# Optimization experiments

Measured on AMD Instinct MI355X. Metric: run time of the kernel, lower is better.

Reference implementation:

```python
import jax, jax.numpy as jnp
import numpy as np


def _gru_cell(xi, h, w_ih, w_hh, b_ih, b_hh):
    # Faithful torch.nn.GRUCell math (as written in KeyedGRU.get_key_gate.one_step)
    gi = xi @ w_ih.T + b_ih            # [B, 3H]
    gh = h @ w_hh.T + b_hh             # [B, 3H]
    i_r, i_i, i_n = jnp.split(gi, 3, axis=1)
    h_r, h_i, h_n = jnp.split(gh, 3, axis=1)
    resetgate = jax.nn.sigmoid(i_r + h_r)
    inputgate = jax.nn.sigmoid(i_i + h_i)
    newgate = jnp.tanh(i_n + resetgate * h_n)
    hy = newgate + inputgate * (h - newgate)
    return hy, resetgate


def setup_inputs() -> dict:
    key = jax.random.key(0)
    ks = jax.random.split(key, 6)
    B, T, I, H = 64, 2048, 256, 256
    KB, KL = 4, 16
    s = 1.0 / float(np.sqrt(H))
    x = jax.random.normal(ks[0], (B, T, I), jnp.float32)
    wm_key = jax.random.normal(ks[1], (KB, KL, I), jnp.float32)
    weight_ih = jax.random.uniform(ks[2], (3 * H, I), jnp.float32, -s, s)
    weight_hh = jax.random.uniform(ks[3], (3 * H, H), jnp.float32, -s, s)
    bias_ih = jax.random.uniform(ks[4], (3 * H,), jnp.float32, -s, s)
    bias_hh = jax.random.uniform(ks[5], (3 * H,), jnp.float32, -s, s)
    return {"x": x, "wm_key": wm_key, "weight_ih": weight_ih,
            "weight_hh": weight_hh, "bias_ih": bias_ih, "bias_hh": bias_hh}


def reference(x, wm_key, weight_ih, weight_hh, bias_ih, bias_hh):
    B, T, I = x.shape
    H = weight_hh.shape[1]
    dt = x.dtype

    # --- key-gate scan (get_key_gate): collect reset gate per key timestep ---
    kt = jnp.transpose(wm_key, (1, 0, 2))          # [KL, KB, I]
    KL, KB, _ = kt.shape
    kh0 = jnp.zeros((KB, H), dt)                   # hidden_init='zero'

    def kstep(h, xi):
        hy, r = _gru_cell(xi, h, weight_ih, weight_hh, bias_ih, bias_hh)
        return hy, r

    _, rgates = jax.lax.scan(kstep, kh0, kt)       # [KL, KB, H]
    gate_means = rgates.mean(axis=1)               # [KL, H] -- key_gates[i].mean(dim=0)
    # pad with ones for steps i >= key_len (no gating applied there)
    gates_full = jnp.concatenate([gate_means, jnp.ones((T - KL, H), dt)], axis=0)  # [T, H]

    # --- main recurrence (teacher_forcing=True, return_sequences=True) ---
    xt = jnp.transpose(x, (1, 0, 2))               # [T, B, I]
    h0 = jnp.zeros((B, H), dt)

    def step(h, inp):
        xi, g = inp
        hy, _ = _gru_cell(xi, h, weight_ih, weight_hh, bias_ih, bias_hh)
        # NOTE: original appends hy to output BEFORE the key-gate multiply,
        # but carries the gated hidden state forward.
        return hy * g, hy

    _, out = jax.lax.scan(step, h0, (xt, gates_full))  # out: [T, B, H]
    return out
```

## Files before the change

kernel.cpp:

```cpp
#include <hip/hip_runtime.h>

typedef _Float16 f16;
typedef _Float16 half8 __attribute__((ext_vector_type(8)));
typedef _Float16 half2v __attribute__((ext_vector_type(2)));
typedef _Float16 half4 __attribute__((ext_vector_type(4)));
typedef float f32x4 __attribute__((ext_vector_type(4)));
typedef unsigned int uint2v __attribute__((ext_vector_type(2)));
typedef unsigned int u32x4v __attribute__((ext_vector_type(4)));

#define G3 768

__global__ void cvt_f32_f16(const float* __restrict__ in, f16* __restrict__ out, int n) {
  int i = blockIdx.x * blockDim.x + threadIdx.x;
  if (i < n) out[i] = (f16)in[i];
}

__global__ __launch_bounds__(256, 2)
void gi_gemm(const float* __restrict__ A, const f16* __restrict__ W,
             const float* __restrict__ b_ih, const float* __restrict__ b_hh,
             f16* __restrict__ GIri, f16* __restrict__ GIn) {
  const int tid = threadIdx.x;
  const int lane = tid & 63;
  const int w = tid >> 6;
  const int quad = lane >> 4;
  const int lq = lane & 15;
  const int m0 = blockIdx.x * 64;

  __shared__ __align__(16) f16 Al[64 * 264];
  __shared__ __align__(16) f16 Bl[48 * 264];

#pragma unroll
  for (int i = 0; i < 16; ++i) {
    int f = i * 256 + tid;
    int row = f >> 6;
    int c4 = f & 63;
    float4 v = ((const float4*)A)[(size_t)(m0 + row) * 64 + c4];
    half4 hv = {(f16)v.x, (f16)v.y, (f16)v.z, (f16)v.w};
    *(half4*)&Al[row * 264 + c4 * 4] = hv;
  }
  __syncthreads();

  half8 af[8];
#pragma unroll
  for (int kc = 0; kc < 8; ++kc)
    af[kc] = *(half8*)&Al[(w * 16 + lq) * 264 + kc * 32 + quad * 8];

  for (int nc = 0; nc < 16; ++nc) {
    __syncthreads();
    int n0 = nc * 48;
#pragma unroll
    for (int i = 0; i < 6; ++i) {
      int f = i * 256 + tid;
      int row = f >> 5;
      int c8 = f & 31;
      half8 v = ((const half8*)(W + (size_t)(n0 + row) * 256))[c8];
      *(half8*)&Bl[row * 264 + c8 * 8] = v;
    }
    __syncthreads();

    f32x4 acc[3] = {};
#pragma unroll
    for (int kc = 0; kc < 8; ++kc) {
#pragma unroll
      for (int nt = 0; nt < 3; ++nt) {
        half8 bf = *(half8*)&Bl[(nt * 16 + lq) * 264 + kc * 32 + quad * 8];
        acc[nt] = __builtin_amdgcn_mfma_f32_16x16x32_f16(af[kc], bf, acc[nt], 0, 0, 0);
      }
    }
#pragma unroll
    for (int nt = 0; nt < 3; ++nt) {
      int n = n0 + nt * 16 + lq;
      float bv = b_ih[n] + (n < 512 ? b_hh[n] : 0.f);
      int g = n >> 8;
      int u = n & 255;
      int ww = u >> 5, lq16 = u & 15, s = (u >> 4) & 1;
#pragma unroll
      for (int r = 0; r < 4; ++r) {
        int m = m0 + w * 16 + quad * 4 + r;
        float val = acc[nt][r] + bv;
        size_t base = ((size_t)m * 8 + ww) * 16 + lq16;
        if (g < 2) GIri[base * 4 + g * 2 + s] = (f16)val;
        else       GIn[base * 2 + s] = (f16)val;
      }
    }
  }
}

__device__ __forceinline__ float sigf(float x) {
  return __builtin_amdgcn_rcpf(1.f + __expf(-x));
}
__device__ __forceinline__ float tanhf_(float x) {
  return 1.f - 2.f * __builtin_amdgcn_rcpf(__expf(2.f * x) + 1.f);
}

#if defined(__has_builtin)
#if __has_builtin(__builtin_amdgcn_fdot2)
#define FD(a, b, c) __builtin_amdgcn_fdot2(a, b, c, false)
#endif
#endif
#ifndef FD
#define FD(a, b, c) ((c) + (float)(a)[0] * (float)(b)[0] + (float)(a)[1] * (float)(b)[1])
#endif

#define MF(af, bw, c) __builtin_amdgcn_mfma_f32_16x16x32_f16(af, bw, c, 0, 0, 0)

#define LOADW(t6, kc) { \
    const float* wr_ = Whh + (size_t)(((t6 >> 1) * 256) + w * 32 + ((t6 & 1) * 16) + lq) * 256 + (kc * 32 + colb); \
    float4 va_ = *(const float4*)wr_; float4 vb_ = *(const float4*)(wr_ + 4); \
    w##t6##kc = (half8){(f16)va_.x, (f16)va_.y, (f16)va_.z, (f16)va_.w, \
                        (f16)vb_.x, (f16)vb_.y, (f16)vb_.z, (f16)vb_.w}; }

#define LOADW_T6(t6) \
  LOADW(t6, 0) LOADW(t6, 1) LOADW(t6, 2) LOADW(t6, 3) \
  LOADW(t6, 4) LOADW(t6, 5) LOADW(t6, 6) LOADW(t6, 7)

#define UNPACK2(u32, lo, hi) { half2v h2_ = __builtin_bit_cast(half2v, (unsigned int)(u32)); \
                               lo = (float)h2_[0]; hi = (float)h2_[1]; }

#define H2(v4, j) __builtin_bit_cast(half2v, (unsigned int)((v4)[j]))

#define NCHUNK(c) { \
    a0 = MF(f##c##_, w0##c, a0); a1 = MF(f##c##_, w1##c, a1); \
    a2 = MF(f##c##_, w2##c, a2); a3 = MF(f##c##_, w3##c, a3); \
    int no_ = nC0 ^ ((c) << 6); \
    half8 n0_ = *(const half8*)((const char*)n_lds + no_); \
    half8 n1_ = *(const half8*)((const char*)n_lds + no_ + 8192); \
    u32x4v hu_ = __builtin_bit_cast(u32x4v, f##c##_); \
    u32x4v nu0_ = __builtin_bit_cast(u32x4v, n0_); \
    u32x4v nu1_ = __builtin_bit_cast(u32x4v, n1_); \
    an0 = FD(H2(hu_, 0), H2(nu0_, 0), an0); an1 = FD(H2(hu_, 0), H2(nu1_, 0), an1); \
    an0 = FD(H2(hu_, 1), H2(nu0_, 1), an0); an1 = FD(H2(hu_, 1), H2(nu1_, 1), an1); \
    an0 = FD(H2(hu_, 2), H2(nu0_, 2), an0); an1 = FD(H2(hu_, 2), H2(nu1_, 2), an1); \
    an0 = FD(H2(hu_, 3), H2(nu0_, 3), an0); an1 = FD(H2(hu_, 3), H2(nu1_, 3), an1); }

#define RED(x) { \
    int t_ = __builtin_amdgcn_ds_swizzle(__builtin_bit_cast(int, x), 0x401F); \
    x += __builtin_bit_cast(float, t_); \
    t_ = __builtin_amdgcn_ds_bpermute(pidx, __builtin_bit_cast(int, x)); \
    x += __builtin_bit_cast(float, t_); }

#define STEP(tcur, PRI, PN) { \
    const f16* hr_ = &hbuf[(tcur) & 1][0]; \
    half8 f0_ = *(const half8*)(hr_ + 0 * 32 + colb); \
    half8 f1_ = *(const half8*)(hr_ + 1 * 32 + colb); \
    half8 f2_ = *(const half8*)(hr_ + 2 * 32 + colb); \
    half8 f3_ = *(const half8*)(hr_ + 3 * 32 + colb); \
    half8 f4_ = *(const half8*)(hr_ + 4 * 32 + colb); \
    half8 f5_ = *(const half8*)(hr_ + 5 * 32 + colb); \
    half8 f6_ = *(const half8*)(hr_ + 6 * 32 + colb); \
    half8 f7_ = *(const half8*)(hr_ + 7 * 32 + colb); \
    float gr0_, gr1_, gi0_, gi1_, gn0_, gn1_; \
    UNPACK2(PRI[0], gr0_, gr1_); \
    UNPACK2(PRI[1], gi0_, gi1_); \
    UNPACK2(PN, gn0_, gn1_); \
    if ((tcur) + 2 < T) { \
      PRI = *(const uint2v*)(gri + (size_t)((tcur) + 2) * 512); \
      PN = *(const unsigned int*)(gn + (size_t)((tcur) + 2) * 256); \
    } \
    f32x4 a0 = {}, a1 = {}, a2 = {}, a3 = {}; \
    float an0 = 0.f, an1 = 0.f; \
    NCHUNK(0) NCHUNK(1) NCHUNK(2) NCHUNK(3) \
    NCHUNK(4) NCHUNK(5) NCHUNK(6) NCHUNK(7) \
    RED(an0) RED(an1) \
    float rg0_ = sigf(gr0_ + a0[0]); \
    float rg1_ = sigf(gr1_ + a1[0]); \
    float ig0_ = sigf(gi0_ + a2[0]); \
    float ig1_ = sigf(gi1_ + a3[0]); \
    float ng0_ = tanhf_(gn0_ + rg0_ * (bn0 + an0)); \
    float ng1_ = tanhf_(gn1_ + rg1_ * (bn1 + an1)); \
    float hy0_ = ng0_ + ig0_ * (h0 - ng0_); \
    float hy1_ = ng1_ + ig1_ * (h1 - ng1_); \
    if (IS_KEY) { \
      if (quad == 0) { float* o_ = out + ((size_t)(tcur) * nb + b) * 256 + u0; o_[0] = rg0_; o_[16] = rg1_; } \
      h0 = hy0_; h1 = hy1_; \
    } else { \
      if (quad == 0) { float* o_ = out + ((size_t)(tcur) * nb + b) * 256 + u0; o_[0] = hy0_; o_[16] = hy1_; } \
      float gm0_ = 1.f, gm1_ = 1.f; \
      if ((tcur) < 16) { gm0_ = gates[(tcur) * 256 + u0]; gm1_ = gates[(tcur) * 256 + u0 + 16]; } \
      h0 = hy0_ * gm0_; h1 = hy1_ * gm1_; \
    } \
    if (quad == 0) { f16* hw_ = &hbuf[((tcur) + 1) & 1][0]; hw_[u0] = (f16)h0; hw_[u0 + 16] = (f16)h1; } \
    __asm__ volatile("" ::: "memory"); \
    __builtin_amdgcn_s_waitcnt(0xC07F);  \
    __builtin_amdgcn_s_barrier(); \
    __asm__ volatile("" ::: "memory"); }

template <bool IS_KEY>
__global__ __launch_bounds__(512)
__attribute__((amdgpu_waves_per_eu(2, 2)))
void gru_scan(const float* __restrict__ Whh, const float* __restrict__ bhh,
              const f16* __restrict__ GIri, const f16* __restrict__ GIn,
              const float* __restrict__ gates, float* __restrict__ out, int T) {
  const int tid = threadIdx.x;
  const int lane = tid & 63;
  const int w = tid >> 6;
  const int quad = lane >> 4;
  const int lq = lane & 15;
  const int b = blockIdx.x;
  const int nb = gridDim.x;
  const int colb = quad * 8;
  const int u0 = w * 32 + lq;
  const int pidx = (lane ^ 32) << 2;

  __shared__ __align__(16) f16 n_lds[256 * 256];
  __shared__ __align__(16) f16 hbuf[2][256];

  half8 w00, w01, w02, w03, w04, w05, w06, w07;
  half8 w10, w11, w12, w13, w14, w15, w16, w17;
  half8 w20, w21, w22, w23, w24, w25, w26, w27;
  half8 w30, w31, w32, w33, w34, w35, w36, w37;
  LOADW_T6(0) LOADW_T6(1) LOADW_T6(2) LOADW_T6(3)

#pragma unroll 4
  for (int i = 0; i < 16; ++i) {
    int gid = i * 512 + tid;
    int rn = gid >> 5, g = gid & 31;
    const float* p_ = Whh + (size_t)(512 + rn) * 256 + g * 8;
    float4 va = *(const float4*)p_;
    float4 vb = *(const float4*)(p_ + 4);
    half8 hv = {(f16)va.x, (f16)va.y, (f16)va.z, (f16)va.w,
                (f16)vb.x, (f16)vb.y, (f16)vb.z, (f16)vb.w};
    *(half8*)((char*)n_lds + rn * 512 + ((g ^ (rn & 7)) << 4)) = hv;
  }

  if (tid < 256) { hbuf[0][tid] = (f16)0.f; hbuf[1][tid] = (f16)0.f; }

  const int e_ = u0 & 7;
  const int nC0 = u0 * 512 + ((quad ^ (e_ & 3)) << 4) + ((e_ >> 2) << 6);

  float h0 = 0.f, h1 = 0.f;
  const float bn0 = bhh[512 + u0];
  const float bn1 = bhh[512 + u0 + 16];

  const size_t mstart = (size_t)b * T;
  const f16* gri = GIri + ((mstart * 8 + w) * 16 + lq) * 4;
  const f16* gn  = GIn + ((mstart * 8 + w) * 16 + lq) * 2;

  uint2v priA = *(const uint2v*)(gri);
  unsigned int pnA = *(const unsigned int*)(gn);
  uint2v priB = *(const uint2v*)(gri + 512);
  unsigned int pnB = *(const unsigned int*)(gn + 256);

  __syncthreads();

  for (int t = 0; t < T; t += 2) {
    STEP(t, priA, pnA)
    STEP(t + 1, priB, pnB)
  }
}

__global__ void gate_mean(const float* __restrict__ rg, float* __restrict__ g) {
  int i = blockIdx.x * 256 + threadIdx.x;
  int l = i >> 8;
  int j = i & 255;
  float s = 0.f;
#pragma unroll
  for (int kb = 0; kb < 4; ++kb) s += rg[((size_t)l * 4 + kb) * 256 + j];
  g[i] = 0.25f * s;
}

extern "C" void kernel_launch(void* const* d_in, const int* in_sizes, int n_in,
                              void* d_out, int out_size, void* d_ws, size_t ws_size,
                              hipStream_t stream) {
  const float* x      = (const float*)d_in[0];
  const float* wm_key = (const float*)d_in[1];
  const float* w_ih   = (const float*)d_in[2];
  const float* w_hh   = (const float*)d_in[3];
  const float* b_ih   = (const float*)d_in[4];
  const float* b_hh   = (const float*)d_in[5];
  float* out = (float*)d_out;

  char* ws = (char*)d_ws;
  const size_t GIRI_OFF  = 0;
  const size_t GIN_OFF   = GIRI_OFF + 134217728ull;
  const size_t WIH_OFF   = GIN_OFF + 67108864ull;
  const size_t GIKRI_OFF = WIH_OFF + 393216ull;
  const size_t GIKN_OFF  = GIKRI_OFF + 65536ull;
  const size_t RG_OFF    = GIKN_OFF + 32768ull;
  const size_t G_OFF     = RG_OFF + 65536ull;
  f16*   GIri  = (f16*)(ws + GIRI_OFF);
  f16*   GIn   = (f16*)(ws + GIN_OFF);
  f16*   Wih   = (f16*)(ws + WIH_OFF);
  f16*   GIkri = (f16*)(ws + GIKRI_OFF);
  f16*   GIkn  = (f16*)(ws + GIKN_OFF);
  float* rg    = (float*)(ws + RG_OFF);
  float* g     = (float*)(ws + G_OFF);

  cvt_f32_f16<<<dim3(768), dim3(256), 0, stream>>>(w_ih, Wih, G3 * 256);
  gi_gemm<<<dim3(2048), dim3(256), 0, stream>>>(x, Wih, b_ih, b_hh, GIri, GIn);
  gi_gemm<<<dim3(1), dim3(256), 0, stream>>>(wm_key, Wih, b_ih, b_hh, GIkri, GIkn);
  gru_scan<true><<<dim3(4), dim3(512), 0, stream>>>(w_hh, b_hh, GIkri, GIkn, g, rg, 16);
  gate_mean<<<dim3(16), dim3(256), 0, stream>>>(rg, g);
  gru_scan<false><<<dim3(64), dim3(512), 0, stream>>>(w_hh, b_hh, GIri, GIn, g, out, 2048);
}
```

Before: 3.503 ms.

## Move input and new-gate recurrent weights into registers, use packed dot products

The update-gate and new-gate parts of W_hh are now held per lane in registers as half2 pairs. They are combined with the hidden state through scalar dot products plus a cross-lane reduction, where before the update gate used MFMA and the new gate was streamed from a 128 KB LDS copy. This drops the LDS weight reads and the large shared allocation, and reduces MFMA work to the reset gate only. The h-fragment loads are also interleaved with the compute chunks. In exchange it adds 128 VGPRs of weights and more VALU dot-product and reduction instructions on the serial per-step critical path.

```diff
diff --git a/kernel.cpp b/kernel.cpp
--- a/kernel.cpp
+++ b/kernel.cpp
@@ -114,24 +114,35 @@
   LOADW(t6, 0) LOADW(t6, 1) LOADW(t6, 2) LOADW(t6, 3) \
   LOADW(t6, 4) LOADW(t6, 5) LOADW(t6, 6) LOADW(t6, 7)
 
+#define LDW2(arr, grow, u) { \
+    _Pragma("unroll") \
+    for (int c_ = 0; c_ < 8; ++c_) { \
+      const float* p_ = Whh + ((size_t)(grow) * 256 + (u)) * 256 + c_ * 32 + colb; \
+      float4 va_ = *(const float4*)p_; \
+      float4 vb_ = *(const float4*)(p_ + 4); \
+      arr[c_ * 4 + 0] = (half2v){(f16)va_.x, (f16)va_.y}; \
+      arr[c_ * 4 + 1] = (half2v){(f16)va_.z, (f16)va_.w}; \
+      arr[c_ * 4 + 2] = (half2v){(f16)vb_.x, (f16)vb_.y}; \
+      arr[c_ * 4 + 3] = (half2v){(f16)vb_.z, (f16)vb_.w}; \
+    } }
+
 #define UNPACK2(u32, lo, hi) { half2v h2_ = __builtin_bit_cast(half2v, (unsigned int)(u32)); \
                                lo = (float)h2_[0]; hi = (float)h2_[1]; }
 
 #define H2(v4, j) __builtin_bit_cast(half2v, (unsigned int)((v4)[j]))
 
-#define NCHUNK(c) { \
+#define CH(c) { \
     a0 = MF(f##c##_, w0##c, a0); a1 = MF(f##c##_, w1##c, a1); \
-    a2 = MF(f##c##_, w2##c, a2); a3 = MF(f##c##_, w3##c, a3); \
-    int no_ = nC0 ^ ((c) << 6); \
-    half8 n0_ = *(const half8*)((const char*)n_lds + no_); \
-    half8 n1_ = *(const half8*)((const char*)n_lds + no_ + 8192); \
     u32x4v hu_ = __builtin_bit_cast(u32x4v, f##c##_); \
-    u32x4v nu0_ = __builtin_bit_cast(u32x4v, n0_); \
-    u32x4v nu1_ = __builtin_bit_cast(u32x4v, n1_); \
-    an0 = FD(H2(hu_, 0), H2(nu0_, 0), an0); an1 = FD(H2(hu_, 0), H2(nu1_, 0), an1); \
-    an0 = FD(H2(hu_, 1), H2(nu0_, 1), an0); an1 = FD(H2(hu_, 1), H2(nu1_, 1), an1); \
-    an0 = FD(H2(hu_, 2), H2(nu0_, 2), an0); an1 = FD(H2(hu_, 2), H2(nu1_, 2), an1); \
-    an0 = FD(H2(hu_, 3), H2(nu0_, 3), an0); an1 = FD(H2(hu_, 3), H2(nu1_, 3), an1); }
+    half2v h20_ = H2(hu_, 0), h21_ = H2(hu_, 1), h22_ = H2(hu_, 2), h23_ = H2(hu_, 3); \
+    ai0 = FD(h20_, wiA[(c) * 4 + 0], ai0); ai1 = FD(h20_, wiB[(c) * 4 + 0], ai1); \
+    an0 = FD(h20_, wnA[(c) * 4 + 0], an0); an1 = FD(h20_, wnB[(c) * 4 + 0], an1); \
+    ai0 = FD(h21_, wiA[(c) * 4 + 1], ai0); ai1 = FD(h21_, wiB[(c) * 4 + 1], ai1); \
+    an0 = FD(h21_, wnA[(c) * 4 + 1], an0); an1 = FD(h21_, wnB[(c) * 4 + 1], an1); \
+    ai0 = FD(h22_, wiA[(c) * 4 + 2], ai0); ai1 = FD(h22_, wiB[(c) * 4 + 2], ai1); \
+    an0 = FD(h22_, wnA[(c) * 4 + 2], an0); an1 = FD(h22_, wnB[(c) * 4 + 2], an1); \
+    ai0 = FD(h23_, wiA[(c) * 4 + 3], ai0); ai1 = FD(h23_, wiB[(c) * 4 + 3], ai1); \
+    an0 = FD(h23_, wnA[(c) * 4 + 3], an0); an1 = FD(h23_, wnB[(c) * 4 + 3], an1); }
 
 #define RED(x) { \
     int t_ = __builtin_amdgcn_ds_swizzle(__builtin_bit_cast(int, x), 0x401F); \
@@ -141,14 +152,22 @@
 
 #define STEP(tcur, PRI, PN) { \
     const f16* hr_ = &hbuf[(tcur) & 1][0]; \
+    f32x4 a0 = {}, a1 = {}; \
+    float ai0 = 0.f, ai1 = 0.f, an0 = 0.f, an1 = 0.f; \
     half8 f0_ = *(const half8*)(hr_ + 0 * 32 + colb); \
     half8 f1_ = *(const half8*)(hr_ + 1 * 32 + colb); \
     half8 f2_ = *(const half8*)(hr_ + 2 * 32 + colb); \
     half8 f3_ = *(const half8*)(hr_ + 3 * 32 + colb); \
+    CH(0) \
     half8 f4_ = *(const half8*)(hr_ + 4 * 32 + colb); \
+    CH(1) \
     half8 f5_ = *(const half8*)(hr_ + 5 * 32 + colb); \
+    CH(2) \
     half8 f6_ = *(const half8*)(hr_ + 6 * 32 + colb); \
+    CH(3) \
     half8 f7_ = *(const half8*)(hr_ + 7 * 32 + colb); \
+    CH(4) CH(5) CH(6) CH(7) \
+    RED(ai0) RED(ai1) RED(an0) RED(an1) \
     float gr0_, gr1_, gi0_, gi1_, gn0_, gn1_; \
     UNPACK2(PRI[0], gr0_, gr1_); \
     UNPACK2(PRI[1], gi0_, gi1_); \
@@ -157,15 +176,10 @@
       PRI = *(const uint2v*)(gri + (size_t)((tcur) + 2) * 512); \
       PN = *(const unsigned int*)(gn + (size_t)((tcur) + 2) * 256); \
     } \
-    f32x4 a0 = {}, a1 = {}, a2 = {}, a3 = {}; \
-    float an0 = 0.f, an1 = 0.f; \
-    NCHUNK(0) NCHUNK(1) NCHUNK(2) NCHUNK(3) \
-    NCHUNK(4) NCHUNK(5) NCHUNK(6) NCHUNK(7) \
-    RED(an0) RED(an1) \
     float rg0_ = sigf(gr0_ + a0[0]); \
     float rg1_ = sigf(gr1_ + a1[0]); \
-    float ig0_ = sigf(gi0_ + a2[0]); \
-    float ig1_ = sigf(gi1_ + a3[0]); \
+    float ig0_ = sigf(gi0_ + ai0); \
+    float ig1_ = sigf(gi1_ + ai1); \
     float ng0_ = tanhf_(gn0_ + rg0_ * (bn0 + an0)); \
     float ng1_ = tanhf_(gn1_ + rg1_ * (bn1 + an1)); \
     float hy0_ = ng0_ + ig0_ * (h0 - ng0_); \
@@ -202,31 +216,17 @@
   const int u0 = w * 32 + lq;
   const int pidx = (lane ^ 32) << 2;
 
-  __shared__ __align__(16) f16 n_lds[256 * 256];
   __shared__ __align__(16) f16 hbuf[2][256];
 
   half8 w00, w01, w02, w03, w04, w05, w06, w07;
   half8 w10, w11, w12, w13, w14, w15, w16, w17;
-  half8 w20, w21, w22, w23, w24, w25, w26, w27;
-  half8 w30, w31, w32, w33, w34, w35, w36, w37;
-  LOADW_T6(0) LOADW_T6(1) LOADW_T6(2) LOADW_T6(3)
-
-#pragma unroll 4
-  for (int i = 0; i < 16; ++i) {
-    int gid = i * 512 + tid;
-    int rn = gid >> 5, g = gid & 31;
-    const float* p_ = Whh + (size_t)(512 + rn) * 256 + g * 8;
-    float4 va = *(const float4*)p_;
-    float4 vb = *(const float4*)(p_ + 4);
-    half8 hv = {(f16)va.x, (f16)va.y, (f16)va.z, (f16)va.w,
-                (f16)vb.x, (f16)vb.y, (f16)vb.z, (f16)vb.w};
-    *(half8*)((char*)n_lds + rn * 512 + ((g ^ (rn & 7)) << 4)) = hv;
-  }
+  LOADW_T6(0) LOADW_T6(1)
+
+  half2v wiA[32], wiB[32], wnA[32], wnB[32];
+  LDW2(wiA, 1, u0) LDW2(wiB, 1, u0 + 16)
+  LDW2(wnA, 2, u0) LDW2(wnB, 2, u0 + 16)
 
   if (tid < 256) { hbuf[0][tid] = (f16)0.f; hbuf[1][tid] = (f16)0.f; }
-
-  const int e_ = u0 & 7;
-  const int nC0 = u0 * 512 + ((quad ^ (e_ & 3)) << 4) + ((e_ >> 2) << 6);
 
   float h0 = 0.f, h1 = 0.f;
   const float bn0 = bhh[512 + u0];
```

Result: slower. 3.691 ms (+5.4%).
